# Optimization experiments

Hardware: AMD Instinct MI355X
Metric: run time of the kernel (lower is better)

The kernel has to match this reference:

```python
import jax, jax.numpy as jnp
import numpy as np

N = 100000
E = 1200000
F_IN = 64
H = 64
PE = 100000
NE = 100000


def setup_inputs() -> dict:
    key = jax.random.key(0)
    ks = jax.random.split(key, 8)
    x = jax.random.normal(ks[0], (N, F_IN), dtype=jnp.float32)
    edge_index = jax.random.randint(ks[1], (2, E), 0, N, dtype=jnp.int64)
    pos_edge_index = jax.random.randint(ks[2], (2, PE), 0, N, dtype=jnp.int64)
    neg_edge_index = jax.random.randint(ks[3], (2, NE), 0, N, dtype=jnp.int64)
    # glorot-ish init for GCNConv linear weights, zero bias (PyG default)
    W1 = jax.random.normal(ks[4], (F_IN, H), dtype=jnp.float32) * (1.0 / np.sqrt(F_IN))
    b1 = jnp.zeros((H,), dtype=jnp.float32)
    W2 = jax.random.normal(ks[5], (H, H), dtype=jnp.float32) * (1.0 / np.sqrt(H))
    b2 = jnp.zeros((H,), dtype=jnp.float32)
    return {"x": x, "edge_index": edge_index, "pos_edge_index": pos_edge_index,
            "neg_edge_index": neg_edge_index, "W1": W1, "b1": b1, "W2": W2, "b2": b2}


def _gcn_norm(edge_index, num_nodes):
    # PyG gcn_norm with add_self_loops=True: deg over col, norm = d^-1/2[row]*d^-1/2[col]
    loop = jnp.arange(num_nodes, dtype=edge_index.dtype)
    src = jnp.concatenate([edge_index[0], loop])
    dst = jnp.concatenate([edge_index[1], loop])
    deg = jax.ops.segment_sum(jnp.ones_like(dst, dtype=jnp.float32), dst,
                              num_segments=num_nodes)
    dis = jnp.where(deg > 0, jax.lax.rsqrt(jnp.maximum(deg, 1.0)), 0.0)
    norm = dis[src] * dis[dst]  # [E+N]
    return src, dst, norm


def _gcn_conv(x, W, b, src, dst, norm, num_nodes):
    h = x @ W                               # [N, H] dense transform first (out_dim small)
    msg = h[src] * norm[:, None]            # gather + scale, [E+N, H]
    out = jax.ops.segment_sum(msg, dst, num_segments=num_nodes)  # scatter-add
    return out + b


def reference(x, edge_index, pos_edge_index, neg_edge_index, W1, b1, W2, b2):
    src, dst, norm = _gcn_norm(edge_index, N)
    z = _gcn_conv(x, W1, b1, src, dst, norm, N)
    z = jax.nn.relu(z)
    z = _gcn_conv(z, W2, b2, src, dst, norm, N)  # [N, H] node embeddings
    # decode: dot product over concatenated pos/neg edge pairs
    ei = jnp.concatenate([pos_edge_index, neg_edge_index], axis=-1)  # [2, PE+NE]
    logits = jnp.sum(z[ei[0]] * z[ei[1]], axis=1)  # [PE+NE]
    return logits
```

## Files before the change

kernel.cpp:

```cpp
#include <hip/hip_runtime.h>

#define NN 100000
#define NE 1200000
#define NPOS 100000
#define NNEG 100000

#define NBUCK ((NN + 255) / 256)
#define BCAP 3712
#define TILE 2048
#define EPT 4

typedef unsigned short bf16_t;

__device__ __forceinline__ float bf2f(bf16_t b) {
    return __uint_as_float(((unsigned int)b) << 16);
}
__device__ __forceinline__ bf16_t f2bf(float f) {
    unsigned int u = __float_as_uint(f);
    u += 0x7FFFu + ((u >> 16) & 1u);
    return (bf16_t)(u >> 16);
}
__device__ __forceinline__ float ulo(unsigned int u) { return bf2f((bf16_t)(u & 0xFFFFu)); }
__device__ __forceinline__ float uhi(unsigned int u) { return bf2f((bf16_t)(u >> 16)); }

__device__ __forceinline__ void acc8(float* a, uint4 u) {
    a[0] += ulo(u.x); a[1] += uhi(u.x);
    a[2] += ulo(u.y); a[3] += uhi(u.y);
    a[4] += ulo(u.z); a[5] += uhi(u.z);
    a[6] += ulo(u.w); a[7] += uhi(u.w);
}

#define GETC(v, i) ((i) == 0 ? (v).x : (i) == 1 ? (v).y : (i) == 2 ? (v).z : (v).w)


__global__ __launch_bounds__(256) void zero_gcur_kernel(int* __restrict__ gcur) {
    int i = blockIdx.x * 256 + threadIdx.x;
    if (i < NBUCK) gcur[i] = 0;
}


__global__ __launch_bounds__(512) void bin_kernel(const int* __restrict__ src,
                                                  const int* __restrict__ dst,
                                                  int* __restrict__ gcur,
                                                  unsigned int* __restrict__ brec) {
    __shared__ int hcnt[NBUCK];
    __shared__ int hbase[NBUCK];
    for (int b = threadIdx.x; b < NBUCK; b += 512) hcnt[b] = 0;
    __syncthreads();

    const int tile0 = blockIdx.x * TILE;
    int bk[EPT];
    int rank[EPT];
    unsigned int rec[EPT];
#pragma unroll
    for (int i = 0; i < EPT; ++i) {
        int e = tile0 + i * 512 + threadIdx.x;
        if (e < NE) {
            int s = src[e];
            int d = dst[e];
            bk[i] = d >> 8;
            rec[i] = ((unsigned int)(d & 255) << 24) | (unsigned int)s;
            rank[i] = atomicAdd(&hcnt[bk[i]], 1);
        } else {
            bk[i] = -1;
        }
    }
    __syncthreads();
    for (int b = threadIdx.x; b < NBUCK; b += 512) {
        int h = hcnt[b];
        if (h > 0) hbase[b] = atomicAdd(&gcur[b], h);
    }
    __syncthreads();
#pragma unroll
    for (int i = 0; i < EPT; ++i) {
        if (bk[i] >= 0) {
            int p = hbase[bk[i]] + rank[i];
            if (p < BCAP) brec[(size_t)bk[i] * BCAP + p] = rec[i];
        }
    }
}


__global__ __launch_bounds__(256) void bucket_csr_kernel(const int* __restrict__ gcur,
                                                         const unsigned int* __restrict__ brec,
                                                         int* __restrict__ csr,
                                                         int* __restrict__ st,
                                                         int* __restrict__ en,
                                                         float* __restrict__ dis) {
    __shared__ int hist[256];
    __shared__ int scanv[256];
    __shared__ int cur[256];
    __shared__ int sorted[BCAP];
    const int b = blockIdx.x;
    const int t = threadIdx.x;
    const int n = min(gcur[b], BCAP);
    const unsigned int* rec = brec + (size_t)b * BCAP;

    hist[t] = 0;
    __syncthreads();
    for (int i = t; i < n; i += 256) atomicAdd(&hist[rec[i] >> 24], 1);
    __syncthreads();

    int c = hist[t];
    scanv[t] = c;
    __syncthreads();
    for (int off = 1; off < 256; off <<= 1) {
        int add = (t >= off) ? scanv[t - off] : 0;
        __syncthreads();
        scanv[t] += add;
        __syncthreads();
    }
    int base = scanv[t] - c;
    cur[t] = base;
    __syncthreads();

    for (int i = t; i < n; i += 256) {
        unsigned int r = rec[i];
        int p = atomicAdd(&cur[r >> 24], 1);
        sorted[p] = (int)(r & 0xFFFFFF);
    }
    __syncthreads();

    for (int i = t; i < n; i += 256) csr[(size_t)b * BCAP + i] = sorted[i];

    int v = b * 256 + t;
    if (v < NN) {
        st[v] = b * BCAP + base;
        en[v] = b * BCAP + base + c;
        dis[v] = rsqrtf((float)(c + 1));
    }
}


__device__ __forceinline__ void gemm_tile_compute(const float4* __restrict__ xs4,
                                                  const float4* __restrict__ ws4,
                                                  int ty, int tx, float acc[4][4]) {
#pragma unroll 2
    for (int k4 = 0; k4 < 16; ++k4) {
        float4 xa0 = xs4[(ty * 4 + 0) * 17 + k4];
        float4 xa1 = xs4[(ty * 4 + 1) * 17 + k4];
        float4 xa2 = xs4[(ty * 4 + 2) * 17 + k4];
        float4 xa3 = xs4[(ty * 4 + 3) * 17 + k4];
        float4 wk0 = ws4[(k4 * 4 + 0) * 16 + tx];
        float4 wk1 = ws4[(k4 * 4 + 1) * 16 + tx];
        float4 wk2 = ws4[(k4 * 4 + 2) * 16 + tx];
        float4 wk3 = ws4[(k4 * 4 + 3) * 16 + tx];
#pragma unroll
        for (int kk = 0; kk < 4; ++kk) {
            float4 wv = (kk == 0) ? wk0 : (kk == 1) ? wk1 : (kk == 2) ? wk2 : wk3;
            float x0 = GETC(xa0, kk), x1 = GETC(xa1, kk);
            float x2 = GETC(xa2, kk), x3 = GETC(xa3, kk);
            acc[0][0] += x0 * wv.x; acc[0][1] += x0 * wv.y; acc[0][2] += x0 * wv.z; acc[0][3] += x0 * wv.w;
            acc[1][0] += x1 * wv.x; acc[1][1] += x1 * wv.y; acc[1][2] += x1 * wv.z; acc[1][3] += x1 * wv.w;
            acc[2][0] += x2 * wv.x; acc[2][1] += x2 * wv.y; acc[2][2] += x2 * wv.z; acc[2][3] += x2 * wv.w;
            acc[3][0] += x3 * wv.x; acc[3][1] += x3 * wv.y; acc[3][2] += x3 * wv.z; acc[3][3] += x3 * wv.w;
        }
    }
}

__global__ __launch_bounds__(256) void gemm64_f32in_kernel(const float* __restrict__ X,
                                                           const float* __restrict__ W,
                                                           const float* __restrict__ dis,
                                                           bf16_t* __restrict__ Hout, int n) {
    __shared__ float4 xs4[64 * 17];
    __shared__ float4 ws4[64 * 16];
    const int tx = threadIdx.x & 15;
    const int ty = threadIdx.x >> 4;
    const int row0 = blockIdx.x * 64;

    const float4* X4 = reinterpret_cast<const float4*>(X + (size_t)row0 * 64);
    const float4* W4 = reinterpret_cast<const float4*>(W);

#pragma unroll
    for (int i = 0; i < 4; ++i) {
        int idx = threadIdx.x + i * 256;
        int r = idx >> 4, c4 = idx & 15;
        int row = row0 + r;
        xs4[r * 17 + c4] = (row < n) ? X4[idx] : make_float4(0.f, 0.f, 0.f, 0.f);
        ws4[idx] = W4[idx];
    }
    __syncthreads();

    float acc[4][4] = {};
    gemm_tile_compute(xs4, ws4, ty, tx, acc);

#pragma unroll
    for (int r = 0; r < 4; ++r) {
        int rw = row0 + ty * 4 + r;
        if (rw < n) {
            float d = dis[rw];
            unsigned int lo = (unsigned int)f2bf(acc[r][0] * d) |
                              ((unsigned int)f2bf(acc[r][1] * d) << 16);
            unsigned int hi = (unsigned int)f2bf(acc[r][2] * d) |
                              ((unsigned int)f2bf(acc[r][3] * d) << 16);
            uint2 u; u.x = lo; u.y = hi;
            *reinterpret_cast<uint2*>(&Hout[(size_t)rw * 64 + tx * 4]) = u;
        }
    }
}


__global__ __launch_bounds__(256) void agg_gemm_kernel(const int* __restrict__ csr,
                                                       const int* __restrict__ st,
                                                       const int* __restrict__ en,
                                                       const float* __restrict__ dis,
                                                       const uint4* __restrict__ Hp8,
                                                       const float* __restrict__ bias,
                                                       const float* __restrict__ W2,
                                                       bf16_t* __restrict__ Hout, int n) {
    __shared__ float4 zs4[32 * 17];
    __shared__ float4 ws4[64 * 16];
    const int lane = threadIdx.x & 63;
    const int g = lane >> 3;
    const int fl = lane & 7;
    const int v0 = blockIdx.x * 32;
    const int lrow = ((threadIdx.x >> 6) << 3) + g;
    int v = v0 + lrow;
    if (v >= n) v = n - 1;

    const float4* W4 = reinterpret_cast<const float4*>(W2);
#pragma unroll
    for (int i = 0; i < 4; ++i) ws4[threadIdx.x + i * 256] = W4[threadIdx.x + i * 256];

    int e = st[v];
    const int e1 = en[v];
    float a0[8] = {}, a1[8] = {}, a2[8] = {}, a3[8] = {};
    acc8(a0, Hp8[(size_t)v * 8 + fl]);

    for (; e + 4 <= e1; e += 4) {
        int s0 = csr[e];
        int s1 = csr[e + 1];
        int s2 = csr[e + 2];
        int s3 = csr[e + 3];
        uint4 u0 = Hp8[(size_t)s0 * 8 + fl];
        uint4 u1 = Hp8[(size_t)s1 * 8 + fl];
        uint4 u2 = Hp8[(size_t)s2 * 8 + fl];
        uint4 u3 = Hp8[(size_t)s3 * 8 + fl];
        acc8(a0, u0);
        acc8(a1, u1);
        acc8(a2, u2);
        acc8(a3, u3);
    }
    for (; e < e1; ++e) acc8(a1, Hp8[(size_t)csr[e] * 8 + fl]);

    {
        float d = dis[v];
        float4 bA = reinterpret_cast<const float4*>(bias)[fl * 2];
        float4 bB = reinterpret_cast<const float4*>(bias)[fl * 2 + 1];
        float4 zA, zB;
        zA.x = fmaxf(((a0[0] + a1[0]) + (a2[0] + a3[0])) * d + bA.x, 0.f);
        zA.y = fmaxf(((a0[1] + a1[1]) + (a2[1] + a3[1])) * d + bA.y, 0.f);
        zA.z = fmaxf(((a0[2] + a1[2]) + (a2[2] + a3[2])) * d + bA.z, 0.f);
        zA.w = fmaxf(((a0[3] + a1[3]) + (a2[3] + a3[3])) * d + bA.w, 0.f);
        zB.x = fmaxf(((a0[4] + a1[4]) + (a2[4] + a3[4])) * d + bB.x, 0.f);
        zB.y = fmaxf(((a0[5] + a1[5]) + (a2[5] + a3[5])) * d + bB.y, 0.f);
        zB.z = fmaxf(((a0[6] + a1[6]) + (a2[6] + a3[6])) * d + bB.z, 0.f);
        zB.w = fmaxf(((a0[7] + a1[7]) + (a2[7] + a3[7])) * d + bB.w, 0.f);
        zs4[lrow * 17 + fl * 2]     = zA;
        zs4[lrow * 17 + fl * 2 + 1] = zB;
    }
    __syncthreads();

    const int tx = threadIdx.x & 15;
    const int ty = threadIdx.x >> 4;
    float acc[2][4] = {};
#pragma unroll 2
    for (int k4 = 0; k4 < 16; ++k4) {
        float4 xa0 = zs4[(ty * 2 + 0) * 17 + k4];
        float4 xa1 = zs4[(ty * 2 + 1) * 17 + k4];
        float4 wk0 = ws4[(k4 * 4 + 0) * 16 + tx];
        float4 wk1 = ws4[(k4 * 4 + 1) * 16 + tx];
        float4 wk2 = ws4[(k4 * 4 + 2) * 16 + tx];
        float4 wk3 = ws4[(k4 * 4 + 3) * 16 + tx];
#pragma unroll
        for (int kk = 0; kk < 4; ++kk) {
            float4 wv = (kk == 0) ? wk0 : (kk == 1) ? wk1 : (kk == 2) ? wk2 : wk3;
            float x0 = GETC(xa0, kk), x1 = GETC(xa1, kk);
            acc[0][0] += x0 * wv.x; acc[0][1] += x0 * wv.y; acc[0][2] += x0 * wv.z; acc[0][3] += x0 * wv.w;
            acc[1][0] += x1 * wv.x; acc[1][1] += x1 * wv.y; acc[1][2] += x1 * wv.z; acc[1][3] += x1 * wv.w;
        }
    }
#pragma unroll
    for (int r = 0; r < 2; ++r) {
        int rw = v0 + ty * 2 + r;
        if (rw < n) {
            float d = dis[rw];
            unsigned int lo = (unsigned int)f2bf(acc[r][0] * d) |
                              ((unsigned int)f2bf(acc[r][1] * d) << 16);
            unsigned int hi = (unsigned int)f2bf(acc[r][2] * d) |
                              ((unsigned int)f2bf(acc[r][3] * d) << 16);
            uint2 u; u.x = lo; u.y = hi;
            *reinterpret_cast<uint2*>(&Hout[(size_t)rw * 64 + tx * 4]) = u;
        }
    }
}


__global__ __launch_bounds__(256) void agg_kernel(const int* __restrict__ csr,
                                                  const int* __restrict__ st,
                                                  const int* __restrict__ en,
                                                  const float* __restrict__ dis,
                                                  const uint4* __restrict__ Hp8,
                                                  const float* __restrict__ bias,
                                                  uint4* __restrict__ Z8, int n) {
    const int lane = threadIdx.x & 63;
    const int g = lane >> 3;
    const int fl = lane & 7;
    int v = blockIdx.x * 32 + ((threadIdx.x >> 6) << 3) + g;
    const bool act = v < n;
    if (!act) v = n - 1;

    int e = st[v];
    const int e1 = en[v];

    float a0[8] = {}, a1[8] = {}, a2[8] = {}, a3[8] = {};
    acc8(a0, Hp8[(size_t)v * 8 + fl]);

    for (; e + 4 <= e1; e += 4) {
        int s0 = csr[e];
        int s1 = csr[e + 1];
        int s2 = csr[e + 2];
        int s3 = csr[e + 3];
        uint4 u0 = Hp8[(size_t)s0 * 8 + fl];
        uint4 u1 = Hp8[(size_t)s1 * 8 + fl];
        uint4 u2 = Hp8[(size_t)s2 * 8 + fl];
        uint4 u3 = Hp8[(size_t)s3 * 8 + fl];
        acc8(a0, u0);
        acc8(a1, u1);
        acc8(a2, u2);
        acc8(a3, u3);
    }
    for (; e < e1; ++e) {
        acc8(a1, Hp8[(size_t)csr[e] * 8 + fl]);
    }

    if (act) {
        float d = dis[v];
        float4 bA = reinterpret_cast<const float4*>(bias)[fl * 2];
        float4 bB = reinterpret_cast<const float4*>(bias)[fl * 2 + 1];
        float z0 = ((a0[0] + a1[0]) + (a2[0] + a3[0])) * d + bA.x;
        float z1 = ((a0[1] + a1[1]) + (a2[1] + a3[1])) * d + bA.y;
        float z2 = ((a0[2] + a1[2]) + (a2[2] + a3[2])) * d + bA.z;
        float z3 = ((a0[3] + a1[3]) + (a2[3] + a3[3])) * d + bA.w;
        float z4 = ((a0[4] + a1[4]) + (a2[4] + a3[4])) * d + bB.x;
        float z5 = ((a0[5] + a1[5]) + (a2[5] + a3[5])) * d + bB.y;
        float z6 = ((a0[6] + a1[6]) + (a2[6] + a3[6])) * d + bB.z;
        float z7 = ((a0[7] + a1[7]) + (a2[7] + a3[7])) * d + bB.w;
        uint4 u;
        u.x = (unsigned int)f2bf(z0) | ((unsigned int)f2bf(z1) << 16);
        u.y = (unsigned int)f2bf(z2) | ((unsigned int)f2bf(z3) << 16);
        u.z = (unsigned int)f2bf(z4) | ((unsigned int)f2bf(z5) << 16);
        u.w = (unsigned int)f2bf(z6) | ((unsigned int)f2bf(z7) << 16);
        Z8[(size_t)v * 8 + fl] = u;
    }
}


__global__ __launch_bounds__(256) void decode_kernel(const int* __restrict__ pos,
                                                     const int* __restrict__ neg,
                                                     const uint4* __restrict__ Z8,
                                                     float* __restrict__ out) {
    const int lane = threadIdx.x & 63;
    const int fl = lane & 7;
    const int pair = blockIdx.x * 32 + ((threadIdx.x >> 6) << 3) + (lane >> 3);
    if (pair >= NPOS + NNEG) return;
    int a, b;
    if (pair < NPOS) {
        a = pos[pair];
        b = pos[NPOS + pair];
    } else {
        int p = pair - NPOS;
        a = neg[p];
        b = neg[NNEG + p];
    }
    uint4 ua = Z8[(size_t)a * 8 + fl];
    uint4 ub = Z8[(size_t)b * 8 + fl];
    float v = ulo(ua.x) * ulo(ub.x) + uhi(ua.x) * uhi(ub.x)
            + ulo(ua.y) * ulo(ub.y) + uhi(ua.y) * uhi(ub.y)
            + ulo(ua.z) * ulo(ub.z) + uhi(ua.z) * uhi(ub.z)
            + ulo(ua.w) * ulo(ub.w) + uhi(ua.w) * uhi(ub.w);
#pragma unroll
    for (int off = 4; off > 0; off >>= 1) v += __shfl_xor(v, off, 64);
    if (fl == 0) out[pair] = v;
}


__global__ __launch_bounds__(256) void init_deg_kernel(float* __restrict__ deg, int n) {
    int i = blockIdx.x * 256 + threadIdx.x;
    if (i < n) deg[i] = 1.0f;
}
__global__ __launch_bounds__(256) void deg_count_kernel(const int* __restrict__ dst,
                                                        float* __restrict__ deg, int e) {
    int i = blockIdx.x * 256 + threadIdx.x;
    if (i < e) atomicAdd(&deg[dst[i]], 1.0f);
}
__global__ __launch_bounds__(256) void dis_kernel(float* __restrict__ deg, int n) {
    int i = blockIdx.x * 256 + threadIdx.x;
    if (i < n) deg[i] = rsqrtf(deg[i]);
}
template <bool RELU>
__global__ __launch_bounds__(256) void gemm64_f32out_kernel(const float* __restrict__ X,
                                                            const float* __restrict__ W,
                                                            float* __restrict__ Hout, int n) {
    __shared__ float xs[64][64];
    const int lane = threadIdx.x & 63;
    const int wid = threadIdx.x >> 6;
    float w[64];
#pragma unroll
    for (int k = 0; k < 64; ++k) w[k] = W[k * 64 + lane];
    const int row0 = blockIdx.x * 64;
#pragma unroll
    for (int i = 0; i < 16; ++i) {
        int idx = threadIdx.x + i * 256;
        int r = idx >> 6, c = idx & 63;
        int row = row0 + r;
        float v = (row < n) ? X[(size_t)row * 64 + c] : 0.0f;
        if (RELU) v = fmaxf(v, 0.0f);
        xs[r][c] = v;
    }
    __syncthreads();
#pragma unroll 1
    for (int rr = 0; rr < 16; ++rr) {
        int r = wid * 16 + rr;
        int row = row0 + r;
        if (row < n) {
            float acc = 0.0f;
#pragma unroll
            for (int k = 0; k < 64; ++k) acc += xs[r][k] * w[k];
            Hout[(size_t)row * 64 + lane] = acc;
        }
    }
}
__global__ __launch_bounds__(256) void selfloop_init_kernel(const float* __restrict__ H,
                                                            const float* __restrict__ dis,
                                                            const float* __restrict__ b,
                                                            float* __restrict__ Z, int n) {
    int i = blockIdx.x * 256 + threadIdx.x;
    if (i < n * 16) {
        int v = i >> 4, c = i & 15;
        float d = dis[v], d2 = d * d;
        float4 h4 = reinterpret_cast<const float4*>(H)[i];
        float4 b4 = reinterpret_cast<const float4*>(b)[c];
        float4 z4;
        z4.x = b4.x + h4.x * d2;
        z4.y = b4.y + h4.y * d2;
        z4.z = b4.z + h4.z * d2;
        z4.w = b4.w + h4.w * d2;
        reinterpret_cast<float4*>(Z)[i] = z4;
    }
}
__global__ __launch_bounds__(256) void edge_agg_kernel(const int* __restrict__ src,
                                                       const int* __restrict__ dst,
                                                       const float* __restrict__ dis,
                                                       const float* __restrict__ H,
                                                       float* __restrict__ Z, int e) {
    const int lane = threadIdx.x & 63;
    const int edge = blockIdx.x * 4 + (threadIdx.x >> 6);
    if (edge < e) {
        int s = src[edge];
        int d = dst[edge];
        float nm = dis[s] * dis[d];
        float v = H[(size_t)s * 64 + lane] * nm;
        atomicAdd(&Z[(size_t)d * 64 + lane], v);
    }
}
__global__ __launch_bounds__(256) void decode_f32_kernel(const int* __restrict__ pos,
                                                         const int* __restrict__ neg,
                                                         const float* __restrict__ Z,
                                                         float* __restrict__ out) {
    const int lane = threadIdx.x & 63;
    const int pair = blockIdx.x * 4 + (threadIdx.x >> 6);
    if (pair >= NPOS + NNEG) return;
    int a, b;
    if (pair < NPOS) {
        a = pos[pair];
        b = pos[NPOS + pair];
    } else {
        int p = pair - NPOS;
        a = neg[p];
        b = neg[NNEG + p];
    }
    float v = Z[(size_t)a * 64 + lane] * Z[(size_t)b * 64 + lane];
#pragma unroll
    for (int off = 32; off > 0; off >>= 1) v += __shfl_down(v, off, 64);
    if (lane == 0) out[pair] = v;
}


extern "C" void kernel_launch(void* const* d_in, const int* in_sizes, int n_in,
                              void* d_out, int out_size, void* d_ws, size_t ws_size,
                              hipStream_t stream) {
    const float* x   = (const float*)d_in[0];
    const int*   ei  = (const int*)d_in[1];
    const int*   pos = (const int*)d_in[2];
    const int*   neg = (const int*)d_in[3];
    const float* W1  = (const float*)d_in[4];
    const float* b1  = (const float*)d_in[5];
    const float* W2  = (const float*)d_in[6];
    const float* b2  = (const float*)d_in[7];
    float* out = (float*)d_out;

    const int* src = ei;
    const int* dst = ei + NE;

    char* ws = (char*)d_ws;
    size_t o = 0;
    auto alloc = [&](size_t bytes) {
        size_t p = o;
        o = (o + bytes + 255) & ~(size_t)255;
        return p;
    };
    float*        dis  = (float*)(ws + alloc((size_t)NN * 4));
    int*          gcur = (int*)(ws + alloc((size_t)NBUCK * 4));
    unsigned int* brec = (unsigned int*)(ws + alloc((size_t)NBUCK * BCAP * 4));
    int*          csr  = (int*)(ws + alloc((size_t)NBUCK * BCAP * 4));
    int*          stA  = (int*)(ws + alloc((size_t)NN * 4));
    int*          enA  = (int*)(ws + alloc((size_t)NN * 4));
    bf16_t*       bufA = (bf16_t*)(ws + alloc((size_t)NN * 64 * 2));
    bf16_t*       bufB = (bf16_t*)(ws + alloc((size_t)NN * 64 * 2));

    if (o <= ws_size) {
        zero_gcur_kernel<<<(NBUCK + 255) / 256, 256, 0, stream>>>(gcur);
        bin_kernel<<<(NE + TILE - 1) / TILE, 512, 0, stream>>>(src, dst, gcur, brec);
        bucket_csr_kernel<<<NBUCK, 256, 0, stream>>>(gcur, brec, csr, stA, enA, dis);

        gemm64_f32in_kernel<<<(NN + 63) / 64, 256, 0, stream>>>(x, W1, dis, bufA, NN);

        agg_gemm_kernel<<<(NN + 31) / 32, 256, 0, stream>>>(csr, stA, enA, dis,
                                                            (const uint4*)bufA, b1, W2,
                                                            bufB, NN);

        agg_kernel<<<(NN + 31) / 32, 256, 0, stream>>>(csr, stA, enA, dis,
                                                       (const uint4*)bufB, b2,
                                                       (uint4*)bufA, NN);

        decode_kernel<<<((NPOS + NNEG) + 31) / 32, 256, 0, stream>>>(pos, neg,
                                                                     (const uint4*)bufA, out);
    } else {
        float* fdis = (float*)ws;
        size_t foff = ((size_t)NN * 4 + 255) / 256 * 256;
        float* fA = (float*)(ws + foff);
        float* fB = fA + (size_t)NN * 64;

        init_deg_kernel<<<(NN + 255) / 256, 256, 0, stream>>>(fdis, NN);
        deg_count_kernel<<<(NE + 255) / 256, 256, 0, stream>>>(dst, fdis, NE);
        dis_kernel<<<(NN + 255) / 256, 256, 0, stream>>>(fdis, NN);

        gemm64_f32out_kernel<false><<<(NN + 63) / 64, 256, 0, stream>>>(x, W1, fA, NN);
        selfloop_init_kernel<<<(NN * 16 + 255) / 256, 256, 0, stream>>>(fA, fdis, b1, fB, NN);
        edge_agg_kernel<<<(NE + 3) / 4, 256, 0, stream>>>(src, dst, fdis, fA, fB, NE);

        gemm64_f32out_kernel<true><<<(NN + 63) / 64, 256, 0, stream>>>(fB, W2, fA, NN);
        selfloop_init_kernel<<<(NN * 16 + 255) / 256, 256, 0, stream>>>(fA, fdis, b2, fB, NN);
        edge_agg_kernel<<<(NE + 3) / 4, 256, 0, stream>>>(src, dst, fdis, fA, fB, NE);

        decode_f32_kernel<<<((NPOS + NNEG) + 3) / 4, 256, 0, stream>>>(pos, neg, fB, out);
    }
}
```

Before: 129.6 us.

## Fuse per-bucket CSR build with first-layer GEMM into one kernel

Merges the bucket CSR construction kernel and the first dense X@W1 GEMM into a single kernel. Each block builds the CSR segment for its 256 nodes, keeps their degree normalisers in shared memory, and then computes the GEMM for those same 256 rows in four 64-row tiles, reusing the shared buffer. This removes one kernel launch and the global round trip for dis. In exchange the grid shrinks from about 1563 to 391 blocks, which cuts parallelism for the GEMM, and the GEMM tiles run serially behind the sort phase.

```diff
diff --git a/kernel.cpp b/kernel.cpp
--- a/kernel.cpp
+++ b/kernel.cpp
@@ -77,57 +77,6 @@
             int p = hbase[bk[i]] + rank[i];
             if (p < BCAP) brec[(size_t)bk[i] * BCAP + p] = rec[i];
         }
-    }
-}
-
-
-__global__ __launch_bounds__(256) void bucket_csr_kernel(const int* __restrict__ gcur,
-                                                         const unsigned int* __restrict__ brec,
-                                                         int* __restrict__ csr,
-                                                         int* __restrict__ st,
-                                                         int* __restrict__ en,
-                                                         float* __restrict__ dis) {
-    __shared__ int hist[256];
-    __shared__ int scanv[256];
-    __shared__ int cur[256];
-    __shared__ int sorted[BCAP];
-    const int b = blockIdx.x;
-    const int t = threadIdx.x;
-    const int n = min(gcur[b], BCAP);
-    const unsigned int* rec = brec + (size_t)b * BCAP;
-
-    hist[t] = 0;
-    __syncthreads();
-    for (int i = t; i < n; i += 256) atomicAdd(&hist[rec[i] >> 24], 1);
-    __syncthreads();
-
-    int c = hist[t];
-    scanv[t] = c;
-    __syncthreads();
-    for (int off = 1; off < 256; off <<= 1) {
-        int add = (t >= off) ? scanv[t - off] : 0;
-        __syncthreads();
-        scanv[t] += add;
-        __syncthreads();
-    }
-    int base = scanv[t] - c;
-    cur[t] = base;
-    __syncthreads();
-
-    for (int i = t; i < n; i += 256) {
-        unsigned int r = rec[i];
-        int p = atomicAdd(&cur[r >> 24], 1);
-        sorted[p] = (int)(r & 0xFFFFFF);
-    }
-    __syncthreads();
-
-    for (int i = t; i < n; i += 256) csr[(size_t)b * BCAP + i] = sorted[i];
-
-    int v = b * 256 + t;
-    if (v < NN) {
-        st[v] = b * BCAP + base;
-        en[v] = b * BCAP + base + c;
-        dis[v] = rsqrtf((float)(c + 1));
     }
 }
 
@@ -158,43 +107,108 @@
     }
 }
 
-__global__ __launch_bounds__(256) void gemm64_f32in_kernel(const float* __restrict__ X,
-                                                           const float* __restrict__ W,
-                                                           const float* __restrict__ dis,
-                                                           bf16_t* __restrict__ Hout, int n) {
-    __shared__ float4 xs4[64 * 17];
-    __shared__ float4 ws4[64 * 16];
-    const int tx = threadIdx.x & 15;
-    const int ty = threadIdx.x >> 4;
-    const int row0 = blockIdx.x * 64;
-
-    const float4* X4 = reinterpret_cast<const float4*>(X + (size_t)row0 * 64);
-    const float4* W4 = reinterpret_cast<const float4*>(W);
-
-#pragma unroll
-    for (int i = 0; i < 4; ++i) {
-        int idx = threadIdx.x + i * 256;
-        int r = idx >> 4, c4 = idx & 15;
-        int row = row0 + r;
-        xs4[r * 17 + c4] = (row < n) ? X4[idx] : make_float4(0.f, 0.f, 0.f, 0.f);
-        ws4[idx] = W4[idx];
+
+__global__ __launch_bounds__(256) void csr_gemm_kernel(const int* __restrict__ gcur,
+                                                       const unsigned int* __restrict__ brec,
+                                                       const float* __restrict__ X,
+                                                       const float* __restrict__ W1,
+                                                       int* __restrict__ csr,
+                                                       int* __restrict__ st,
+                                                       int* __restrict__ en,
+                                                       float* __restrict__ dis,
+                                                       bf16_t* __restrict__ Hout) {
+    __shared__ __align__(16) char smraw[64 * 16 * 16 + 64 * 17 * 16];
+    __shared__ float disLoc[256];
+
+    const int b = blockIdx.x;
+    const int t = threadIdx.x;
+
+    {
+        int* hist   = (int*)smraw;
+        int* scanv  = (int*)(smraw + 1024);
+        int* cur    = (int*)(smraw + 2048);
+        int* sorted = (int*)(smraw + 3072);
+
+        const int n = min(gcur[b], BCAP);
+        const unsigned int* rec = brec + (size_t)b * BCAP;
+
+        hist[t] = 0;
+        __syncthreads();
+        for (int i = t; i < n; i += 256) atomicAdd(&hist[rec[i] >> 24], 1);
+        __syncthreads();
+
+        int c = hist[t];
+        scanv[t] = c;
+        __syncthreads();
+        for (int off = 1; off < 256; off <<= 1) {
+            int add = (t >= off) ? scanv[t - off] : 0;
+            __syncthreads();
+            scanv[t] += add;
+            __syncthreads();
+        }
+        int base = scanv[t] - c;
+        cur[t] = base;
+        __syncthreads();
+
+        for (int i = t; i < n; i += 256) {
+            unsigned int r = rec[i];
+            int p = atomicAdd(&cur[r >> 24], 1);
+            sorted[p] = (int)(r & 0xFFFFFF);
+        }
+        __syncthreads();
+
+        for (int i = t; i < n; i += 256) csr[(size_t)b * BCAP + i] = sorted[i];
+
+        float dv = rsqrtf((float)(c + 1));
+        disLoc[t] = dv;
+        int v = b * 256 + t;
+        if (v < NN) {
+            st[v] = b * BCAP + base;
+            en[v] = b * BCAP + base + c;
+            dis[v] = dv;
+        }
     }
     __syncthreads();
 
-    float acc[4][4] = {};
-    gemm_tile_compute(xs4, ws4, ty, tx, acc);
-
-#pragma unroll
-    for (int r = 0; r < 4; ++r) {
-        int rw = row0 + ty * 4 + r;
-        if (rw < n) {
-            float d = dis[rw];
-            unsigned int lo = (unsigned int)f2bf(acc[r][0] * d) |
-                              ((unsigned int)f2bf(acc[r][1] * d) << 16);
-            unsigned int hi = (unsigned int)f2bf(acc[r][2] * d) |
-                              ((unsigned int)f2bf(acc[r][3] * d) << 16);
-            uint2 u; u.x = lo; u.y = hi;
-            *reinterpret_cast<uint2*>(&Hout[(size_t)rw * 64 + tx * 4]) = u;
+    float4* ws4 = (float4*)smraw;
+    float4* xs4 = (float4*)(smraw + 64 * 16 * 16);
+
+    const float4* W4 = reinterpret_cast<const float4*>(W1);
+#pragma unroll
+    for (int i = 0; i < 4; ++i) ws4[t + i * 256] = W4[t + i * 256];
+
+    const int tx = t & 15;
+    const int ty = t >> 4;
+
+#pragma unroll 1
+    for (int tile = 0; tile < 4; ++tile) {
+        const int row0 = b * 256 + tile * 64;
+        const float4* X4 = reinterpret_cast<const float4*>(X + (size_t)row0 * 64);
+        __syncthreads();
+#pragma unroll
+        for (int i = 0; i < 4; ++i) {
+            int idx = t + i * 256;
+            int r = idx >> 4, c4 = idx & 15;
+            int row = row0 + r;
+            xs4[r * 17 + c4] = (row < NN) ? X4[idx] : make_float4(0.f, 0.f, 0.f, 0.f);
+        }
+        __syncthreads();
+
+        float acc[4][4] = {};
+        gemm_tile_compute(xs4, ws4, ty, tx, acc);
+
+#pragma unroll
+        for (int r = 0; r < 4; ++r) {
+            int rw = row0 + ty * 4 + r;
+            if (rw < NN) {
+                float d = disLoc[tile * 64 + ty * 4 + r];
+                unsigned int lo = (unsigned int)f2bf(acc[r][0] * d) |
+                                  ((unsigned int)f2bf(acc[r][1] * d) << 16);
+                unsigned int hi = (unsigned int)f2bf(acc[r][2] * d) |
+                                  ((unsigned int)f2bf(acc[r][3] * d) << 16);
+                uint2 u; u.x = lo; u.y = hi;
+                *reinterpret_cast<uint2*>(&Hout[(size_t)rw * 64 + tx * 4]) = u;
+            }
         }
     }
 }
@@ -522,9 +536,9 @@
     if (o <= ws_size) {
         zero_gcur_kernel<<<(NBUCK + 255) / 256, 256, 0, stream>>>(gcur);
         bin_kernel<<<(NE + TILE - 1) / TILE, 512, 0, stream>>>(src, dst, gcur, brec);
-        bucket_csr_kernel<<<NBUCK, 256, 0, stream>>>(gcur, brec, csr, stA, enA, dis);
-
-        gemm64_f32in_kernel<<<(NN + 63) / 64, 256, 0, stream>>>(x, W1, dis, bufA, NN);
+
+        csr_gemm_kernel<<<NBUCK, 256, 0, stream>>>(gcur, brec, x, W1,
+                                                   csr, stA, enA, dis, bufA);
 
         agg_gemm_kernel<<<(NN + 31) / 32, 256, 0, stream>>>(csr, stA, enA, dis,
                                                             (const uint4*)bufA, b1, W2,
```

Result: slower. 132.4 us (+2.2%).
